# Performance work log

Measured on AMD Instinct MI355X. Metric: run time of the kernel, lower is better.

The kernel has to match this reference:

```python
import jax, jax.numpy as jnp
import numpy as np
from jax import lax

NAG = 3          # hardcoded in the torch module (query slices, catted_torches)
B = 4096         # batch_size per agent
H = 128          # hidden_dim
HEADS = 8
AD = H // HEADS  # attend_dim
STATE, ACT, SCAN = 48, 2, 256
OUTF, HID = 10, 256
NFEAT = 32 * (SCAN - 6)  # conv output features (two VALID convs: k5 then k3)
EPS = 1e-5

def leaky(x):
    return jnp.where(x >= 0, x, 0.01 * x)

def setup_inputs() -> dict:
    key = jax.random.key(0)
    ks = iter(jax.random.split(key, 40))
    def rn(shape, scale=0.05):
        return jax.random.normal(next(ks), shape, dtype=jnp.float32) * scale
    return {
        'obs':  jax.random.normal(next(ks), (NAG * B, STATE), jnp.float32),
        'acts': jax.random.normal(next(ks), (NAG * B, ACT), jnp.float32),
        'scan': jax.random.normal(next(ks), (NAG * B, SCAN), jnp.float32),
        'conv_w1': rn((32, 1, 5)),  'conv_b1': jnp.zeros((32,), jnp.float32),
        'conv_w2': rn((32, 32, 3)), 'conv_b2': jnp.zeros((32,), jnp.float32),
        'fc_w1': rn((256, NFEAT), 0.01), 'fc_b1': jnp.zeros((256,), jnp.float32),
        'fc_w2': rn((OUTF, 256)),        'fc_b2': jnp.zeros((OUTF,), jnp.float32),
        'enc_w': rn((H, STATE + ACT + OUTF)), 'enc_b': jnp.zeros((H,), jnp.float32),
        'Wk': rn((HEADS, AD, H)),
        'Wv': rn((HEADS, AD, H)), 'bv': jnp.zeros((HEADS, AD), jnp.float32),
        'Wq': rn((NAG, HEADS, AD, H)),
        'q1_w1': rn((HID, 2 * H)), 'q1_b1': jnp.zeros((HID,), jnp.float32),
        'q1_w2': rn((HID, HID)),   'q1_b2': jnp.zeros((HID,), jnp.float32),
        'q1_w3': rn((1, HID)),     'q1_b3': jnp.zeros((1,), jnp.float32),
        'q2_w1': rn((HID, 2 * H)), 'q2_b1': jnp.zeros((HID,), jnp.float32),
        'q2_w2': rn((HID, HID)),   'q2_b2': jnp.zeros((HID,), jnp.float32),
        'q2_w3': rn((1, HID)),     'q2_b3': jnp.zeros((1,), jnp.float32),
    }

def reference(obs, acts, scan, conv_w1, conv_b1, conv_w2, conv_b2,
              fc_w1, fc_b1, fc_w2, fc_b2, enc_w, enc_b, Wk, Wv, bv, Wq,
              q1_w1, q1_b1, q1_w2, q1_b2, q1_w3, q1_b3,
              q2_w1, q2_b1, q2_w2, q2_b2, q2_w3, q2_b3):
    dn = ('NCH', 'OIH', 'NCH')
    x = scan[:, None, :]                                            # [N,1,L]
    x = lax.conv_general_dilated(x, conv_w1, (1,), 'VALID', dimension_numbers=dn)
    x = jax.nn.relu(x + conv_b1[None, :, None])
    x = lax.conv_general_dilated(x, conv_w2, (1,), 'VALID', dimension_numbers=dn)
    x = jax.nn.relu(x + conv_b2[None, :, None])
    x = x.reshape(x.shape[0], -1)                                   # [N, NFEAT]
    x = jax.nn.relu(x @ fc_w1.T + fc_b1)
    feats = x @ fc_w2.T + fc_b2                                     # [N, OUTF]

    inps = jnp.concatenate([obs, acts, feats], axis=1)
    mu, var = inps.mean(0), inps.var(0)                             # BatchNorm1d (train, no affine)
    normed = (inps - mu) / jnp.sqrt(var + EPS)
    sa = leaky(normed @ enc_w.T + enc_b).reshape(NAG, B, H)         # [ag,B,H]

    keys = jnp.einsum('gbh,ndh->ngbd', sa, Wk)                      # [hd,ag,B,ad]
    vals = leaky(jnp.einsum('gbh,ndh->ngbd', sa, Wv) + bv[:, None, None, :])
    q = jnp.einsum('gbh,gndh->gnbd', sa, Wq)                        # [ag,hd,B,ad]

    logits = jnp.einsum('gnbd,nobd->gnbo', q, keys) / np.sqrt(AD)   # [ag,hd,B,ag]
    self_mask = jnp.eye(NAG, dtype=bool)[:, None, None, :]          # exclude own agent
    logits = jnp.where(self_mask, -jnp.inf, logits)
    w = jax.nn.softmax(logits, axis=-1)
    other = jnp.einsum('gnbo,nobd->gnbd', w, vals)                  # [ag,hd,B,ad]
    other = other.transpose(0, 2, 1, 3).reshape(NAG, B, H)          # heads concatenated

    emb = jnp.concatenate([sa, other], axis=2).reshape(NAG * B, 2 * H)

    def mlp(x, w1, b1, w2, b2, w3, b3):
        x = jax.nn.relu(x @ w1.T + b1)
        x = jax.nn.relu(x @ w2.T + b2)
        return x @ w3.T + b3

    q1 = mlp(emb, q1_w1, q1_b1, q1_w2, q1_b2, q1_w3, q1_b3)
    q2 = mlp(emb, q2_w1, q2_b1, q2_w2, q2_b2, q2_w3, q2_b3)
    return (q1, q2)
```

## Files before the change

### kernel.cpp

```cpp
#include <hip/hip_runtime.h>
#include <hip/hip_bf16.h>
#include <cstdint>
#include <cstddef>

typedef unsigned short u16;
typedef __attribute__((ext_vector_type(8))) __bf16 bf16x8;
typedef __attribute__((ext_vector_type(4))) float f32x4;

__device__ __forceinline__ u16 f2b(float f) {
  __hip_bfloat16 h = __float2bfloat16(f);
  return *reinterpret_cast<u16*>(&h);
}
__device__ __forceinline__ uint32_t pk2(float a, float b) {
  __hip_bfloat162 h = __float22bfloat162_rn(make_float2(a, b));
  return *reinterpret_cast<uint32_t*>(&h);
}
__device__ __forceinline__ float b2f(u16 u) {
  union { float f; uint32_t i; } x; x.i = ((uint32_t)u) << 16; return x.f;
}
__device__ __forceinline__ f32x4 mfma16(bf16x8 a, bf16x8 b, f32x4 c) {
  return __builtin_amdgcn_mfma_f32_16x16x32_bf16(a, b, c, 0, 0, 0);
}
__device__ __forceinline__ void async16(const void* g, void* l) {
  __builtin_amdgcn_global_load_lds((const __attribute__((address_space(1))) uint32_t*)g,
                                   (__attribute__((address_space(3))) uint32_t*)l, 16, 0, 0);
}

__global__ __launch_bounds__(256) void w1_perm(const float* __restrict__ w,
                                               u16* __restrict__ o) {
  __shared__ float L[8000];
  int j = blockIdx.x, tid = threadIdx.x;
  for (int i = tid; i < 8000; i += 256) L[i] = w[(size_t)j * 8000 + i];
  __syncthreads();
  for (int i = tid; i < 8000; i += 256) {
    int tt = i >> 5, c2 = i & 31;
    o[(size_t)j * 8000 + i] = f2b(L[c2 * 250 + tt]);
  }
}

struct CvtArgs {
  const float* src[13];
  void* dst[13];
  int cum[14];
  int kind[13];
};
__global__ __launch_bounds__(256) void f2b_multi(CvtArgs a, float* stats) {
  int i = blockIdx.x * 256 + threadIdx.x;
  if (blockIdx.x == 0 && threadIdx.x < 128) stats[threadIdx.x] = 0.f;
  int seg = 0;
  #pragma unroll
  for (int s = 1; s < 13; ++s) if (i >= a.cum[s]) seg = s;
  if (i < a.cum[13]) {
    int off = i - a.cum[seg];
    int kind = a.kind[seg];
    const float* src = a.src[seg];
    if (kind == 0) {
      ((u16*)a.dst[seg])[off] = f2b(src[off]);
    } else if (kind == 1) {
      int c2 = off / 96, rem = off - c2 * 96, kk = rem >> 5, c1 = rem & 31;
      ((u16*)a.dst[seg])[off] = f2b(src[(c2 * 32 + c1) * 3 + kk]);
    } else if (kind == 2) {
      int c1 = off >> 5, k = off & 31;
      ((u16*)a.dst[seg])[off] = f2b(k < 5 ? src[c1 * 5 + k] : 0.f);
    } else {
      ((float*)a.dst[seg])[off] = src[off];
    }
  }
}

__global__ __launch_bounds__(256) void conv_fused(
    const float* __restrict__ scan, const u16* __restrict__ w1g,
    const float* __restrict__ cb1, const u16* __restrict__ w2g,
    const float* __restrict__ cb2, u16* __restrict__ x, int row0) {
  __shared__ float s[260];
  __shared__ __align__(16) u16 A1[256 * 40];
  __shared__ __align__(16) u16 h1T[258 * 40];
  int tid = threadIdx.x;
  int lane = tid & 63, wv = tid >> 6;
  int l15 = lane & 15, quad = lane >> 4;
  s[tid] = scan[(size_t)(row0 + blockIdx.x) * 256 + tid];
  if (tid < 4) s[256 + tid] = 0.f;
  if (tid < 80) h1T[256 * 40 + tid] = 0;
  bf16x8 w1f[2];
  w1f[0] = *(const bf16x8*)&w1g[l15 * 32 + quad * 8];
  w1f[1] = *(const bf16x8*)&w1g[(16 + l15) * 32 + quad * 8];
  bf16x8 w2f[2][3];
  #pragma unroll
  for (int i = 0; i < 2; ++i)
    #pragma unroll
    for (int kk = 0; kk < 3; ++kk)
      w2f[i][kk] = *(const bf16x8*)&w2g[(i * 16 + l15) * 96 + kk * 32 + quad * 8];
  float cb1v[2][4], cb2v[2][4];
  #pragma unroll
  for (int i = 0; i < 2; ++i)
    #pragma unroll
    for (int r = 0; r < 4; ++r) {
      cb1v[i][r] = cb1[i * 16 + quad * 4 + r];
      cb2v[i][r] = cb2[i * 16 + quad * 4 + r];
    }
  __syncthreads();
  {
    union { bf16x8 v; u16 u[8]; } pk;
    #pragma unroll
    for (int k = 0; k < 5; ++k) pk.u[k] = f2b(s[tid + k]);
    pk.u[5] = 0; pk.u[6] = 0; pk.u[7] = 0;
    *(bf16x8*)&A1[tid * 40] = pk.v;
    uint4 z = make_uint4(0, 0, 0, 0);
    *(uint4*)&A1[tid * 40 + 8] = z;
    *(uint4*)&A1[tid * 40 + 16] = z;
    *(uint4*)&A1[tid * 40 + 24] = z;
  }
  __syncthreads();
  f32x4 zero = {0.f, 0.f, 0.f, 0.f};
  {
    f32x4 acc1[4][2];
    #pragma unroll
    for (int nt = 0; nt < 4; ++nt) { acc1[nt][0] = zero; acc1[nt][1] = zero; }
    #pragma unroll
    for (int nt = 0; nt < 4; ++nt) {
      int p = (wv * 4 + nt) * 16 + l15;
      bf16x8 bfr = *(const bf16x8*)&A1[p * 40 + quad * 8];
      acc1[nt][0] = mfma16(w1f[0], bfr, acc1[nt][0]);
      acc1[nt][1] = mfma16(w1f[1], bfr, acc1[nt][1]);
    }
    #pragma unroll
    for (int nt = 0; nt < 4; ++nt) {
      int p = (wv * 4 + nt) * 16 + l15;
      #pragma unroll
      for (int mt = 0; mt < 2; ++mt) {
        float v0 = fmaxf(acc1[nt][mt][0] + cb1v[mt][0], 0.f);
        float v1 = fmaxf(acc1[nt][mt][1] + cb1v[mt][1], 0.f);
        float v2 = fmaxf(acc1[nt][mt][2] + cb1v[mt][2], 0.f);
        float v3 = fmaxf(acc1[nt][mt][3] + cb1v[mt][3], 0.f);
        uint2 u; u.x = pk2(v0, v1); u.y = pk2(v2, v3);
        *(uint2*)&h1T[p * 40 + mt * 16 + quad * 4] = u;
      }
    }
  }
  __syncthreads();
  f32x4 acc2[4][2];
  #pragma unroll
  for (int jj = 0; jj < 4; ++jj) { acc2[jj][0] = zero; acc2[jj][1] = zero; }
  #pragma unroll
  for (int kk = 0; kk < 3; ++kk) {
    #pragma unroll
    for (int jj = 0; jj < 4; ++jj) {
      int t = (wv * 4 + jj) * 16 + l15 + kk;
      bf16x8 h = *(const bf16x8*)&h1T[t * 40 + quad * 8];
      acc2[jj][0] = mfma16(w2f[0][kk], h, acc2[jj][0]);
      acc2[jj][1] = mfma16(w2f[1][kk], h, acc2[jj][1]);
    }
  }
  u16* xr = x + (size_t)blockIdx.x * 8000;
  #pragma unroll
  for (int jj = 0; jj < 4; ++jj) {
    int t = (wv * 4 + jj) * 16 + l15;
    if (t < 250) {
      #pragma unroll
      for (int i = 0; i < 2; ++i) {
        float v0 = fmaxf(acc2[jj][i][0] + cb2v[i][0], 0.f);
        float v1 = fmaxf(acc2[jj][i][1] + cb2v[i][1], 0.f);
        float v2 = fmaxf(acc2[jj][i][2] + cb2v[i][2], 0.f);
        float v3 = fmaxf(acc2[jj][i][3] + cb2v[i][3], 0.f);
        uint2 u; u.x = pk2(v0, v1); u.y = pk2(v2, v3);
        *(uint2*)&xr[t * 32 + i * 16 + quad * 4] = u;
      }
    }
  }
}

template <int MODE>
__global__ __launch_bounds__(256) void gemm_bt(
    const u16* __restrict__ A, int lda, const u16* __restrict__ W, int ldw,
    const float* __restrict__ bias, float* __restrict__ outF,
    u16* __restrict__ outB, int ldo, int nst, int wq_sel, int a_sel,
    size_t out_zoff) {
  __shared__ __align__(16) u16 As[2][128 * 64];
  __shared__ __align__(16) u16 Bs[2][128 * 64];
  int tid = threadIdx.x;
  int m0 = blockIdx.y * 128, n0 = blockIdx.x * 128;
  if (wq_sel) W += (size_t)(blockIdx.y >> 5) * wq_sel;
  if (a_sel) A += (size_t)(blockIdx.x >> 1) * a_sel;
  int kbase = blockIdx.z * nst * 64;
  if (MODE == 0) outF += (size_t)blockIdx.z * out_zoff;
  const u16* Ap = A + (size_t)m0 * lda + kbase;
  const u16* Wp = W + (size_t)n0 * ldw + kbase;
  int lane = tid & 63, wv = tid >> 6;
  int l15 = lane & 15, quad = lane >> 4;
  int wm = (wv >> 1) * 64, wn = (wv & 1) * 64;
  f32x4 zero = {0.f, 0.f, 0.f, 0.f};
  f32x4 acc[4][4];
  #pragma unroll
  for (int i = 0; i < 4; ++i)
    #pragma unroll
    for (int j = 0; j < 4; ++j) acc[i][j] = zero;

  int srow[4], soff[4], sdst[4];
  #pragma unroll
  for (int it = 0; it < 4; ++it) {
    int c = it * 256 + tid;
    int row = c >> 3, slot = c & 7;
    srow[it] = row;
    soff[it] = ((slot ^ (row & 7)) * 8);
    sdst[it] = c * 8;
  }
  int rslot[2];
  rslot[0] = ((quad ^ (l15 & 7)) * 8);
  rslot[1] = (((4 + quad) ^ (l15 & 7)) * 8);

  #pragma unroll 1
  for (int st = 0; st < nst; ++st) {
    if (st == 0) {
      #pragma unroll
      for (int it = 0; it < 4; ++it) {
        async16(Ap + (size_t)srow[it] * lda + soff[it], &As[0][sdst[it]]);
        async16(Wp + (size_t)srow[it] * ldw + soff[it], &Bs[0][sdst[it]]);
      }
    }
    __syncthreads();
    if (st + 1 < nst) {
      const u16* An = Ap + (st + 1) * 64;
      const u16* Wn = Wp + (st + 1) * 64;
      u16* Ad = &As[(st + 1) & 1][0];
      u16* Bd = &Bs[(st + 1) & 1][0];
      #pragma unroll
      for (int it = 0; it < 4; ++it) {
        async16(An + (size_t)srow[it] * lda + soff[it], Ad + sdst[it]);
        async16(Wn + (size_t)srow[it] * ldw + soff[it], Bd + sdst[it]);
      }
    }
    const u16* Ab = &As[st & 1][0];
    const u16* Bb = &Bs[st & 1][0];
    #pragma unroll
    for (int s = 0; s < 2; ++s) {
      bf16x8 af[4], bfr[4];
      #pragma unroll
      for (int i = 0; i < 4; ++i)
        af[i] = *(const bf16x8*)&Ab[(wm + i * 16 + l15) * 64 + rslot[s]];
      #pragma unroll
      for (int j = 0; j < 4; ++j)
        bfr[j] = *(const bf16x8*)&Bb[(wn + j * 16 + l15) * 64 + rslot[s]];
      #pragma unroll
      for (int i = 0; i < 4; ++i)
        #pragma unroll
        for (int j = 0; j < 4; ++j) acc[i][j] = mfma16(af[i], bfr[j], acc[i][j]);
    }
  }
  #pragma unroll
  for (int i = 0; i < 4; ++i) {
    int mb = m0 + wm + i * 16 + quad * 4;
    #pragma unroll
    for (int j = 0; j < 4; ++j) {
      int n = n0 + wn + j * 16 + l15;
      float bv_ = (MODE == 1 || MODE == 2) ? bias[n] : 0.f;
      #pragma unroll
      for (int r = 0; r < 4; ++r) {
        float v = acc[i][j][r];
        if (MODE == 0) {
          outF[(size_t)(mb + r) * ldo + n] = v;
        } else {
          v += bv_;
          if (MODE == 1) v = fmaxf(v, 0.f);
          if (MODE == 2) v = v >= 0.f ? v : 0.01f * v;
          outB[(size_t)(mb + r) * ldo + n] = f2b(v);
        }
      }
    }
  }
}

__global__ __launch_bounds__(256) void fc2_stats(
    const float* __restrict__ hparts, const float* __restrict__ b1,
    const float* __restrict__ w2, const float* __restrict__ b2,
    const float* __restrict__ obs, const float* __restrict__ acts,
    float* __restrict__ inps, float* __restrict__ stats) {
  __shared__ float hL[32 * 260];
  __shared__ float w2L[10 * 260];
  __shared__ float b1L[256];
  __shared__ float ipL[32 * 61];
  int tid = threadIdx.x, r0 = blockIdx.x * 32;
  b1L[tid] = b1[tid];
  for (int i = tid; i < 2560; i += 256) w2L[(i >> 8) * 260 + (i & 255)] = w2[i];
  for (int i = tid; i < 32 * 48; i += 256) {
    int r = i / 48, f = i - r * 48;
    ipL[r * 61 + f] = obs[(size_t)(r0 + r) * 48 + f];
  }
  if (tid < 64) {
    int r = tid >> 1, f = tid & 1;
    ipL[r * 61 + 48 + f] = acts[(size_t)(r0 + r) * 2 + f];
  }
  __syncthreads();
  const size_t HS = (size_t)12288 * 256;
  for (int i = tid; i < 32 * 256; i += 256) {
    int r = i >> 8, c = i & 255;
    size_t g = (size_t)(r0 + r) * 256 + c;
    float v = b1L[c] + hparts[g] + hparts[g + HS] + hparts[g + 2 * HS] +
              hparts[g + 3 * HS] + hparts[g + 4 * HS];
    hL[r * 260 + c] = fmaxf(v, 0.f);
  }
  __syncthreads();
  {
    int r = tid >> 3, ob = tid & 7;
    for (int o = ob; o < 10; o += 8) {
      float a = 0.f;
      #pragma unroll 8
      for (int c = 0; c < 256; ++c) a += hL[r * 260 + c] * w2L[o * 260 + c];
      ipL[r * 61 + 50 + o] = a + b2[o];
    }
  }
  __syncthreads();
  for (int i = tid; i < 32 * 60; i += 256) {
    int r = i / 60, f = i - r * 60;
    inps[(size_t)(r0 + r) * 64 + f] = ipL[r * 61 + f];
  }
  if (tid < 60) {
    float s = 0.f, s2 = 0.f;
    for (int r = 0; r < 32; ++r) {
      float v = ipL[r * 61 + tid];
      s += v; s2 += v * v;
    }
    atomicAdd(&stats[tid], s);
    atomicAdd(&stats[64 + tid], s2);
  }
}

__global__ __launch_bounds__(256) void enc_kernel(
    const float* __restrict__ inps, const float* __restrict__ stats,
    const float* __restrict__ enc_w, const float* __restrict__ enc_b,
    u16* __restrict__ sab) {
  __shared__ float ewL[128 * 61];
  __shared__ float nrm[32 * 61];
  __shared__ float ebL[128];
  __shared__ float muL[60], ivL[60];
  int tid = threadIdx.x, r0 = blockIdx.x * 32;
  if (tid < 128) ebL[tid] = enc_b[tid];
  if (tid < 60) {
    float s = stats[tid], s2 = stats[64 + tid];
    float mu = s * (1.f / 12288.f);
    float var = s2 * (1.f / 12288.f) - mu * mu;
    muL[tid] = mu;
    ivL[tid] = rsqrtf(var + 1e-5f);
  }
  for (int i = tid; i < 128 * 60; i += 256) {
    int h = i / 60, f = i - h * 60;
    ewL[h * 61 + f] = enc_w[i];
  }
  __syncthreads();
  for (int i = tid; i < 32 * 60; i += 256) {
    int r = i / 60, f = i - r * 60;
    nrm[r * 61 + f] = (inps[(size_t)(r0 + r) * 64 + f] - muL[f]) * ivL[f];
  }
  __syncthreads();
  for (int i = tid; i < 32 * 128; i += 256) {
    int r = i >> 7, h = i & 127;
    float a = ebL[h];
    #pragma unroll 4
    for (int f = 0; f < 60; ++f) a += nrm[r * 61 + f] * ewL[h * 61 + f];
    a = a >= 0.f ? a : 0.01f * a;
    sab[(size_t)(r0 + r) * 128 + h] = f2b(a);
  }
}

__global__ __launch_bounds__(128) void attn_combine(
    const u16* __restrict__ qb, const u16* __restrict__ keysb,
    const u16* __restrict__ valsb, const u16* __restrict__ sab,
    u16* __restrict__ emb) {
  __shared__ float qL[3][128], kL[3][128], vL[3][128];
  __shared__ float lg[3][8][3], wgt[3][8][3];
  int b = blockIdx.x, t = threadIdx.x;
  #pragma unroll
  for (int o = 0; o < 3; ++o) {
    size_t base = (size_t)(o * 4096 + b) * 128 + t;
    qL[o][t] = b2f(qb[base]);
    kL[o][t] = b2f(keysb[base]);
    vL[o][t] = b2f(valsb[base]);
  }
  __syncthreads();
  if (t < 72) {
    int g = t / 24, n = (t / 3) % 8, o = t % 3;
    float a = 0.f;
    #pragma unroll
    for (int d = 0; d < 16; ++d) a += qL[g][n * 16 + d] * kL[o][n * 16 + d];
    lg[g][n][o] = (o == g) ? -1e30f : a * 0.25f;
  }
  __syncthreads();
  if (t < 24) {
    int g = t / 8, n = t % 8;
    float m = fmaxf(fmaxf(lg[g][n][0], lg[g][n][1]), lg[g][n][2]);
    float e0 = expf(lg[g][n][0] - m), e1 = expf(lg[g][n][1] - m),
          e2 = expf(lg[g][n][2] - m);
    float inv = 1.f / (e0 + e1 + e2);
    wgt[g][n][0] = e0 * inv; wgt[g][n][1] = e1 * inv; wgt[g][n][2] = e2 * inv;
  }
  __syncthreads();
  int n = t >> 4, d = t & 15;
  #pragma unroll
  for (int g = 0; g < 3; ++g) {
    float o_ = wgt[g][n][0] * vL[0][n * 16 + d] +
               wgt[g][n][1] * vL[1][n * 16 + d] +
               wgt[g][n][2] * vL[2][n * 16 + d];
    size_t rbase = (size_t)(g * 4096 + b) * 256;
    emb[rbase + 128 + t] = f2b(o_);
    emb[rbase + t] = sab[(size_t)(g * 4096 + b) * 128 + t];
  }
}

__global__ __launch_bounds__(256) void final_dot(
    const u16* __restrict__ t2ab, const float* __restrict__ w3a,
    const float* __restrict__ b3a, const float* __restrict__ w3b,
    const float* __restrict__ b3b, float* __restrict__ out) {
  int wv = threadIdx.x >> 6, lane = threadIdx.x & 63;
  int row = blockIdx.x * 4 + wv;
  float sa_ = 0.f, sb_ = 0.f;
  #pragma unroll
  for (int e = 0; e < 4; ++e) {
    int c = lane * 4 + e;
    sa_ += b2f(t2ab[(size_t)row * 512 + c]) * w3a[c];
    sb_ += b2f(t2ab[(size_t)row * 512 + 256 + c]) * w3b[c];
  }
  #pragma unroll
  for (int off = 32; off; off >>= 1) {
    sa_ += __shfl_down(sa_, off);
    sb_ += __shfl_down(sb_, off);
  }
  if (lane == 0) {
    out[row] = sa_ + b3a[0];
    out[12288 + row] = sb_ + b3b[0];
  }
}

extern "C" void kernel_launch(void* const* d_in, const int* in_sizes, int n_in,
                              void* d_out, int out_size, void* d_ws,
                              size_t ws_size, hipStream_t stream) {
  const float* obs  = (const float*)d_in[0];
  const float* acts = (const float*)d_in[1];
  const float* scan = (const float*)d_in[2];
  const float* cw1  = (const float*)d_in[3];
  const float* cb1  = (const float*)d_in[4];
  const float* cw2  = (const float*)d_in[5];
  const float* cb2  = (const float*)d_in[6];
  const float* fw1  = (const float*)d_in[7];
  const float* fb1  = (const float*)d_in[8];
  const float* fw2  = (const float*)d_in[9];
  const float* fb2  = (const float*)d_in[10];
  const float* encw = (const float*)d_in[11];
  const float* encb = (const float*)d_in[12];
  const float* Wk   = (const float*)d_in[13];
  const float* Wv   = (const float*)d_in[14];
  const float* bv   = (const float*)d_in[15];
  const float* Wq   = (const float*)d_in[16];
  const float* q1w1 = (const float*)d_in[17];
  const float* q1b1 = (const float*)d_in[18];
  const float* q1w2 = (const float*)d_in[19];
  const float* q1b2 = (const float*)d_in[20];
  const float* q1w3 = (const float*)d_in[21];
  const float* q1b3 = (const float*)d_in[22];
  const float* q2w1 = (const float*)d_in[23];
  const float* q2b1 = (const float*)d_in[24];
  const float* q2w2 = (const float*)d_in[25];
  const float* q2b2 = (const float*)d_in[26];
  const float* q2w3 = (const float*)d_in[27];
  const float* q2b3 = (const float*)d_in[28];
  float* out = (float*)d_out;
  char* ws = (char*)d_ws;
  if (ws_size < 166016000u) return;

  u16*   x     = (u16*)(ws + 0);
  u16*   w1b   = (u16*)(ws + 98304000);
  float* hpart = (float*)(ws + 102400000);
  float* stats = (float*)(ws + 165314560);
  u16*   wkb   = (u16*)(ws + 165315584);
  u16*   wvb   = (u16*)(ws + 165348352);
  u16*   wqb   = (u16*)(ws + 165381120);
  u16*   m1ab  = (u16*)(ws + 165479424);
  u16*   m2ab  = (u16*)(ws + 165741568);
  u16*   w2g   = (u16*)(ws + 166003712);
  u16*   w1g   = (u16*)(ws + 166009856);
  float* bc1   = (float*)(ws + 166011904);
  float* bc2   = (float*)(ws + 166013952);
  float* inps  = (float*)(ws + 0);
  u16*   sab   = (u16*)(ws + 3145728);
  u16*   keysb = (u16*)(ws + 6291456);
  u16*   valsb = (u16*)(ws + 9437184);
  u16*   qb    = (u16*)(ws + 12582912);
  u16*   embb  = (u16*)(ws + 15728640);
  u16*   t1ab  = (u16*)(ws + 22020096);
  u16*   t2ab  = (u16*)(ws + 34603008);

  w1_perm<<<256, 256, 0, stream>>>(fw1, w1b);
  CvtArgs ca;
  const float* srcs[13] = {Wk, Wv, Wq, q1w1, q2w1, q1w2, q2w2, cw2, cw1,
                           q1b1, q2b1, q1b2, q2b2};
  void* dsts[13] = {wkb, wvb, wqb, m1ab, m1ab + 65536, m2ab, m2ab + 65536,
                    w2g, w1g, bc1, bc1 + 256, bc2, bc2 + 256};
  const int sz[13] = {16384, 16384, 49152, 65536, 65536, 65536, 65536,
                      3072, 1024, 256, 256, 256, 256};
  const int kinds[13] = {0, 0, 0, 0, 0, 0, 0, 1, 2, 3, 3, 3, 3};
  int cum = 0;
  ca.cum[0] = 0;
  for (int i = 0; i < 13; ++i) {
    ca.src[i] = srcs[i]; ca.dst[i] = dsts[i]; ca.kind[i] = kinds[i];
    cum += sz[i]; ca.cum[i + 1] = cum;
  }
  f2b_multi<<<(cum + 255) / 256, 256, 0, stream>>>(ca, stats);

  for (int s = 0; s < 2; ++s) {
    conv_fused<<<6144, 256, 0, stream>>>(scan, w1g, cb1, w2g, cb2, x, s * 6144);
    gemm_bt<0><<<dim3(2, 48, 5), 256, 0, stream>>>(
        x, 8000, w1b, 8000, nullptr, hpart + (size_t)s * 6144 * 256, nullptr,
        256, 25, 0, 0, (size_t)12288 * 256);
  }
  fc2_stats<<<384, 256, 0, stream>>>(hpart, fb1, fw2, fb2, obs, acts, inps, stats);
  enc_kernel<<<384, 256, 0, stream>>>(inps, stats, encw, encb, sab);
  gemm_bt<3><<<dim3(1, 96, 1), 256, 0, stream>>>(sab, 128, wkb, 128, nullptr,
                                                 nullptr, keysb, 128, 2, 0, 0, 0);
  gemm_bt<2><<<dim3(1, 96, 1), 256, 0, stream>>>(sab, 128, wvb, 128, bv, nullptr,
                                                 valsb, 128, 2, 0, 0, 0);
  gemm_bt<3><<<dim3(1, 96, 1), 256, 0, stream>>>(sab, 128, wqb, 128, nullptr,
                                                 nullptr, qb, 128, 2, 16384, 0, 0);
  attn_combine<<<4096, 128, 0, stream>>>(qb, keysb, valsb, sab, embb);
  gemm_bt<1><<<dim3(4, 96, 1), 256, 0, stream>>>(embb, 256, m1ab, 256, bc1,
                                                 nullptr, t1ab, 512, 4, 0, 0, 0);
  gemm_bt<1><<<dim3(4, 96, 1), 256, 0, stream>>>(t1ab, 512, m2ab, 256, bc2,
                                                 nullptr, t2ab, 512, 4, 0, 256, 0);
  final_dot<<<3072, 256, 0, stream>>>(t2ab, q1w3, q1b3, q2w3, q2b3, out);
}
```

Baseline: 358.2 us.

## Halve GEMM K-tile to 32 and slim conv LDS staging with zero buffer

The shared GEMM kernel's K-stage shrinks from 64 to 32, halving LDS use (64KB to 32KB per block) with a matching swizzle, and every launch's stage count is doubled to cover the same K. This should allow more blocks per CU, in exchange for twice as many barriers and loop iterations per tile. The conv kernel drops its float staging buffer and padded A1 layout. Each thread now reads its five scan taps straight from global memory, and lanes with quad>0 read a shared zero row, which removes two __syncthreads and the zero-fill stores. The conv change relies on wave-local LDS visibility, ordered only by an s_waitcnt, since each wave reads only the A1 rows it wrote itself.

```diff
diff --git a/kernel.cpp b/kernel.cpp
--- a/kernel.cpp
+++ b/kernel.cpp
@@ -72,14 +72,25 @@
     const float* __restrict__ scan, const u16* __restrict__ w1g,
     const float* __restrict__ cb1, const u16* __restrict__ w2g,
     const float* __restrict__ cb2, u16* __restrict__ x, int row0) {
-  __shared__ float s[260];
-  __shared__ __align__(16) u16 A1[256 * 40];
+  __shared__ __align__(16) u16 A1[256 * 8];
+  __shared__ __align__(16) u16 zbuf[4 * 8];
   __shared__ __align__(16) u16 h1T[258 * 40];
   int tid = threadIdx.x;
   int lane = tid & 63, wv = tid >> 6;
   int l15 = lane & 15, quad = lane >> 4;
-  s[tid] = scan[(size_t)(row0 + blockIdx.x) * 256 + tid];
-  if (tid < 4) s[256 + tid] = 0.f;
+  const float* srow = scan + (size_t)(row0 + blockIdx.x) * 256;
+  float sv[5];
+  #pragma unroll
+  for (int k = 0; k < 5; ++k) {
+    int p = tid + k;
+    sv[k] = (p < 256) ? srow[p] : 0.f;
+  }
+  union { bf16x8 v; u16 u[8]; } pk_;
+  #pragma unroll
+  for (int k = 0; k < 5; ++k) pk_.u[k] = f2b(sv[k]);
+  pk_.u[5] = 0; pk_.u[6] = 0; pk_.u[7] = 0;
+  *(bf16x8*)&A1[tid * 8] = pk_.v;
+  if (lane < 8) zbuf[wv * 8 + lane] = 0;
   if (tid < 80) h1T[256 * 40 + tid] = 0;
   bf16x8 w1f[2];
   w1f[0] = *(const bf16x8*)&w1g[l15 * 32 + quad * 8];
@@ -98,19 +109,7 @@
       cb1v[i][r] = cb1[i * 16 + quad * 4 + r];
       cb2v[i][r] = cb2[i * 16 + quad * 4 + r];
     }
-  __syncthreads();
-  {
-    union { bf16x8 v; u16 u[8]; } pk;
-    #pragma unroll
-    for (int k = 0; k < 5; ++k) pk.u[k] = f2b(s[tid + k]);
-    pk.u[5] = 0; pk.u[6] = 0; pk.u[7] = 0;
-    *(bf16x8*)&A1[tid * 40] = pk.v;
-    uint4 z = make_uint4(0, 0, 0, 0);
-    *(uint4*)&A1[tid * 40 + 8] = z;
-    *(uint4*)&A1[tid * 40 + 16] = z;
-    *(uint4*)&A1[tid * 40 + 24] = z;
-  }
-  __syncthreads();
+  asm volatile("s_waitcnt lgkmcnt(0)" ::: "memory");
   f32x4 zero = {0.f, 0.f, 0.f, 0.f};
   {
     f32x4 acc1[4][2];
@@ -119,7 +118,8 @@
     #pragma unroll
     for (int nt = 0; nt < 4; ++nt) {
       int p = (wv * 4 + nt) * 16 + l15;
-      bf16x8 bfr = *(const bf16x8*)&A1[p * 40 + quad * 8];
+      const u16* bp = (quad == 0) ? &A1[p * 8] : &zbuf[wv * 8];
+      bf16x8 bfr = *(const bf16x8*)bp;
       acc1[nt][0] = mfma16(w1f[0], bfr, acc1[nt][0]);
       acc1[nt][1] = mfma16(w1f[1], bfr, acc1[nt][1]);
     }
@@ -175,13 +175,13 @@
     const float* __restrict__ bias, float* __restrict__ outF,
     u16* __restrict__ outB, int ldo, int nst, int wq_sel, int a_sel,
     size_t out_zoff) {
-  __shared__ __align__(16) u16 As[2][128 * 64];
-  __shared__ __align__(16) u16 Bs[2][128 * 64];
+  __shared__ __align__(16) u16 As[2][128 * 32];
+  __shared__ __align__(16) u16 Bs[2][128 * 32];
   int tid = threadIdx.x;
   int m0 = blockIdx.y * 128, n0 = blockIdx.x * 128;
   if (wq_sel) W += (size_t)(blockIdx.y >> 5) * wq_sel;
   if (a_sel) A += (size_t)(blockIdx.x >> 1) * a_sel;
-  int kbase = blockIdx.z * nst * 64;
+  int kbase = blockIdx.z * nst * 32;
   if (MODE == 0) outF += (size_t)blockIdx.z * out_zoff;
   const u16* Ap = A + (size_t)m0 * lda + kbase;
   const u16* Wp = W + (size_t)n0 * ldw + kbase;
@@ -195,56 +195,51 @@
     #pragma unroll
     for (int j = 0; j < 4; ++j) acc[i][j] = zero;
 
-  int srow[4], soff[4], sdst[4];
-  #pragma unroll
-  for (int it = 0; it < 4; ++it) {
+  int srow[2], soff[2], sdst[2];
+  #pragma unroll
+  for (int it = 0; it < 2; ++it) {
     int c = it * 256 + tid;
-    int row = c >> 3, slot = c & 7;
+    int row = c >> 2, slot = c & 3;
     srow[it] = row;
-    soff[it] = ((slot ^ (row & 7)) * 8);
+    soff[it] = ((slot ^ (row & 3)) * 8);
     sdst[it] = c * 8;
   }
-  int rslot[2];
-  rslot[0] = ((quad ^ (l15 & 7)) * 8);
-  rslot[1] = (((4 + quad) ^ (l15 & 7)) * 8);
+  int rslot = ((quad ^ (l15 & 3)) * 8);
 
   #pragma unroll 1
   for (int st = 0; st < nst; ++st) {
     if (st == 0) {
       #pragma unroll
-      for (int it = 0; it < 4; ++it) {
+      for (int it = 0; it < 2; ++it) {
         async16(Ap + (size_t)srow[it] * lda + soff[it], &As[0][sdst[it]]);
         async16(Wp + (size_t)srow[it] * ldw + soff[it], &Bs[0][sdst[it]]);
       }
     }
     __syncthreads();
     if (st + 1 < nst) {
-      const u16* An = Ap + (st + 1) * 64;
-      const u16* Wn = Wp + (st + 1) * 64;
+      const u16* An = Ap + (st + 1) * 32;
+      const u16* Wn = Wp + (st + 1) * 32;
       u16* Ad = &As[(st + 1) & 1][0];
       u16* Bd = &Bs[(st + 1) & 1][0];
       #pragma unroll
-      for (int it = 0; it < 4; ++it) {
+      for (int it = 0; it < 2; ++it) {
         async16(An + (size_t)srow[it] * lda + soff[it], Ad + sdst[it]);
         async16(Wn + (size_t)srow[it] * ldw + soff[it], Bd + sdst[it]);
       }
     }
     const u16* Ab = &As[st & 1][0];
     const u16* Bb = &Bs[st & 1][0];
-    #pragma unroll
-    for (int s = 0; s < 2; ++s) {
-      bf16x8 af[4], bfr[4];
+    bf16x8 af[4], bfr[4];
+    #pragma unroll
+    for (int i = 0; i < 4; ++i)
+      af[i] = *(const bf16x8*)&Ab[(wm + i * 16 + l15) * 32 + rslot];
+    #pragma unroll
+    for (int j = 0; j < 4; ++j)
+      bfr[j] = *(const bf16x8*)&Bb[(wn + j * 16 + l15) * 32 + rslot];
+    #pragma unroll
+    for (int i = 0; i < 4; ++i)
       #pragma unroll
-      for (int i = 0; i < 4; ++i)
-        af[i] = *(const bf16x8*)&Ab[(wm + i * 16 + l15) * 64 + rslot[s]];
-      #pragma unroll
-      for (int j = 0; j < 4; ++j)
-        bfr[j] = *(const bf16x8*)&Bb[(wn + j * 16 + l15) * 64 + rslot[s]];
-      #pragma unroll
-      for (int i = 0; i < 4; ++i)
-        #pragma unroll
-        for (int j = 0; j < 4; ++j) acc[i][j] = mfma16(af[i], bfr[j], acc[i][j]);
-    }
+      for (int j = 0; j < 4; ++j) acc[i][j] = mfma16(af[i], bfr[j], acc[i][j]);
   }
   #pragma unroll
   for (int i = 0; i < 4; ++i) {
@@ -508,20 +503,20 @@
     conv_fused<<<6144, 256, 0, stream>>>(scan, w1g, cb1, w2g, cb2, x, s * 6144);
     gemm_bt<0><<<dim3(2, 48, 5), 256, 0, stream>>>(
         x, 8000, w1b, 8000, nullptr, hpart + (size_t)s * 6144 * 256, nullptr,
-        256, 25, 0, 0, (size_t)12288 * 256);
+        256, 50, 0, 0, (size_t)12288 * 256);
   }
   fc2_stats<<<384, 256, 0, stream>>>(hpart, fb1, fw2, fb2, obs, acts, inps, stats);
   enc_kernel<<<384, 256, 0, stream>>>(inps, stats, encw, encb, sab);
   gemm_bt<3><<<dim3(1, 96, 1), 256, 0, stream>>>(sab, 128, wkb, 128, nullptr,
-                                                 nullptr, keysb, 128, 2, 0, 0, 0);
+                                                 nullptr, keysb, 128, 4, 0, 0, 0);
   gemm_bt<2><<<dim3(1, 96, 1), 256, 0, stream>>>(sab, 128, wvb, 128, bv, nullptr,
-                                                 valsb, 128, 2, 0, 0, 0);
+                                                 valsb, 128, 4, 0, 0, 0);
   gemm_bt<3><<<dim3(1, 96, 1), 256, 0, stream>>>(sab, 128, wqb, 128, nullptr,
-                                                 nullptr, qb, 128, 2, 16384, 0, 0);
+                                                 nullptr, qb, 128, 4, 16384, 0, 0);
   attn_combine<<<4096, 128, 0, stream>>>(qb, keysb, valsb, sab, embb);
   gemm_bt<1><<<dim3(4, 96, 1), 256, 0, stream>>>(embb, 256, m1ab, 256, bc1,
-                                                 nullptr, t1ab, 512, 4, 0, 0, 0);
+                                                 nullptr, t1ab, 512, 8, 0, 0, 0);
   gemm_bt<1><<<dim3(4, 96, 1), 256, 0, stream>>>(t1ab, 512, m2ab, 256, bc2,
-                                                 nullptr, t2ab, 512, 4, 0, 256, 0);
+                                                 nullptr, t2ab, 512, 8, 0, 256, 0);
   final_dot<<<3072, 256, 0, stream>>>(t2ab, q1w3, q1b3, q2w3, q2b3, out);
 }
```

New measurement: 380.8 us. 1.06x slower.

## Restructure conv kernel per-wave rows, fuse K/V/Q GEMMs, use 64-row GEMM tiles

Applied to the files above, without the earlier changes.

The conv kernel now gives each wave its own 64-position slice, with private LDS and no block barriers, and loops over 4 rows per block. It also reads scan directly from global memory and feeds the K=32 MFMA from a shared zero buffer for the padded quads. The conv and fc1 GEMM now run over all 12288 rows in one pass instead of two halves, which doubles the workspace. The K, V and Q projections are merged into one launch (MODE 4), and every GEMM uses 64-row M tiles so more blocks are in flight, at the cost of less reuse per block.

```diff
diff --git a/kernel.cpp b/kernel.cpp
--- a/kernel.cpp
+++ b/kernel.cpp
@@ -71,16 +71,12 @@
 __global__ __launch_bounds__(256) void conv_fused(
     const float* __restrict__ scan, const u16* __restrict__ w1g,
     const float* __restrict__ cb1, const u16* __restrict__ w2g,
-    const float* __restrict__ cb2, u16* __restrict__ x, int row0) {
-  __shared__ float s[260];
-  __shared__ __align__(16) u16 A1[256 * 40];
-  __shared__ __align__(16) u16 h1T[258 * 40];
-  int tid = threadIdx.x;
-  int lane = tid & 63, wv = tid >> 6;
+    const float* __restrict__ cb2, u16* __restrict__ x) {
+  __shared__ __align__(16) u16 A1[4][80 * 8];
+  __shared__ __align__(16) u16 zb[4][8];
+  __shared__ __align__(16) u16 h1[4][80 * 40];
+  int tid = threadIdx.x, lane = tid & 63, wv = tid >> 6;
   int l15 = lane & 15, quad = lane >> 4;
-  s[tid] = scan[(size_t)(row0 + blockIdx.x) * 256 + tid];
-  if (tid < 4) s[256 + tid] = 0.f;
-  if (tid < 80) h1T[256 * 40 + tid] = 0;
   bf16x8 w1f[2];
   w1f[0] = *(const bf16x8*)&w1g[l15 * 32 + quad * 8];
   w1f[1] = *(const bf16x8*)&w1g[(16 + l15) * 32 + quad * 8];
@@ -98,34 +94,53 @@
       cb1v[i][r] = cb1[i * 16 + quad * 4 + r];
       cb2v[i][r] = cb2[i * 16 + quad * 4 + r];
     }
-  __syncthreads();
-  {
-    union { bf16x8 v; u16 u[8]; } pk;
-    #pragma unroll
-    for (int k = 0; k < 5; ++k) pk.u[k] = f2b(s[tid + k]);
-    pk.u[5] = 0; pk.u[6] = 0; pk.u[7] = 0;
-    *(bf16x8*)&A1[tid * 40] = pk.v;
-    uint4 z = make_uint4(0, 0, 0, 0);
-    *(uint4*)&A1[tid * 40 + 8] = z;
-    *(uint4*)&A1[tid * 40 + 16] = z;
-    *(uint4*)&A1[tid * 40 + 24] = z;
-  }
-  __syncthreads();
+  if (lane < 8) zb[wv][lane] = 0;
+  u16* A1w = &A1[wv][0];
+  u16* h1w = &h1[wv][0];
+  int p0 = wv * 64;
   f32x4 zero = {0.f, 0.f, 0.f, 0.f};
-  {
-    f32x4 acc1[4][2];
-    #pragma unroll
-    for (int nt = 0; nt < 4; ++nt) { acc1[nt][0] = zero; acc1[nt][1] = zero; }
-    #pragma unroll
-    for (int nt = 0; nt < 4; ++nt) {
-      int p = (wv * 4 + nt) * 16 + l15;
-      bf16x8 bfr = *(const bf16x8*)&A1[p * 40 + quad * 8];
+  #pragma unroll 1
+  for (int rr = 0; rr < 4; ++rr) {
+    int row = blockIdx.x * 4 + rr;
+    const float* srow = scan + (size_t)row * 256;
+    asm volatile("s_waitcnt lgkmcnt(0)" ::: "memory");
+    {
+      union { bf16x8 v; u16 u[8]; } pk_;
+      int gp = p0 + lane;
+      #pragma unroll
+      for (int k = 0; k < 5; ++k) {
+        int p = gp + k;
+        pk_.u[k] = f2b(p < 256 ? srow[p] : 0.f);
+      }
+      pk_.u[5] = 0; pk_.u[6] = 0; pk_.u[7] = 0;
+      *(bf16x8*)&A1w[lane * 8] = pk_.v;
+      if (lane < 16) {
+        union { bf16x8 v; u16 u[8]; } pq_;
+        gp = p0 + 64 + lane;
+        #pragma unroll
+        for (int k = 0; k < 5; ++k) {
+          int p = gp + k;
+          pq_.u[k] = f2b(p < 256 ? srow[p] : 0.f);
+        }
+        pq_.u[5] = 0; pq_.u[6] = 0; pq_.u[7] = 0;
+        *(bf16x8*)&A1w[(64 + lane) * 8] = pq_.v;
+      }
+    }
+    asm volatile("s_waitcnt lgkmcnt(0)" ::: "memory");
+    f32x4 acc1[5][2];
+    #pragma unroll
+    for (int nt = 0; nt < 5; ++nt) { acc1[nt][0] = zero; acc1[nt][1] = zero; }
+    #pragma unroll
+    for (int nt = 0; nt < 5; ++nt) {
+      int lr = nt * 16 + l15;
+      const u16* bp = (quad == 0) ? &A1w[lr * 8] : &zb[wv][0];
+      bf16x8 bfr = *(const bf16x8*)bp;
       acc1[nt][0] = mfma16(w1f[0], bfr, acc1[nt][0]);
       acc1[nt][1] = mfma16(w1f[1], bfr, acc1[nt][1]);
     }
     #pragma unroll
-    for (int nt = 0; nt < 4; ++nt) {
-      int p = (wv * 4 + nt) * 16 + l15;
+    for (int nt = 0; nt < 5; ++nt) {
+      int lr = nt * 16 + l15;
       #pragma unroll
       for (int mt = 0; mt < 2; ++mt) {
         float v0 = fmaxf(acc1[nt][mt][0] + cb1v[mt][0], 0.f);
@@ -133,53 +148,59 @@
         float v2 = fmaxf(acc1[nt][mt][2] + cb1v[mt][2], 0.f);
         float v3 = fmaxf(acc1[nt][mt][3] + cb1v[mt][3], 0.f);
         uint2 u; u.x = pk2(v0, v1); u.y = pk2(v2, v3);
-        *(uint2*)&h1T[p * 40 + mt * 16 + quad * 4] = u;
+        *(uint2*)&h1w[lr * 40 + mt * 16 + quad * 4] = u;
       }
     }
-  }
-  __syncthreads();
-  f32x4 acc2[4][2];
-  #pragma unroll
-  for (int jj = 0; jj < 4; ++jj) { acc2[jj][0] = zero; acc2[jj][1] = zero; }
-  #pragma unroll
-  for (int kk = 0; kk < 3; ++kk) {
+    asm volatile("s_waitcnt lgkmcnt(0)" ::: "memory");
+    f32x4 acc2[4][2];
+    #pragma unroll
+    for (int jj = 0; jj < 4; ++jj) { acc2[jj][0] = zero; acc2[jj][1] = zero; }
+    #pragma unroll
+    for (int kk = 0; kk < 3; ++kk) {
+      #pragma unroll
+      for (int jj = 0; jj < 4; ++jj) {
+        int lt = jj * 16 + l15 + kk;
+        bf16x8 h = *(const bf16x8*)&h1w[lt * 40 + quad * 8];
+        acc2[jj][0] = mfma16(w2f[0][kk], h, acc2[jj][0]);
+        acc2[jj][1] = mfma16(w2f[1][kk], h, acc2[jj][1]);
+      }
+    }
+    u16* xr = x + (size_t)row * 8000;
     #pragma unroll
     for (int jj = 0; jj < 4; ++jj) {
-      int t = (wv * 4 + jj) * 16 + l15 + kk;
-      bf16x8 h = *(const bf16x8*)&h1T[t * 40 + quad * 8];
-      acc2[jj][0] = mfma16(w2f[0][kk], h, acc2[jj][0]);
-      acc2[jj][1] = mfma16(w2f[1][kk], h, acc2[jj][1]);
-    }
-  }
-  u16* xr = x + (size_t)blockIdx.x * 8000;
-  #pragma unroll
-  for (int jj = 0; jj < 4; ++jj) {
-    int t = (wv * 4 + jj) * 16 + l15;
-    if (t < 250) {
-      #pragma unroll
-      for (int i = 0; i < 2; ++i) {
-        float v0 = fmaxf(acc2[jj][i][0] + cb2v[i][0], 0.f);
-        float v1 = fmaxf(acc2[jj][i][1] + cb2v[i][1], 0.f);
-        float v2 = fmaxf(acc2[jj][i][2] + cb2v[i][2], 0.f);
-        float v3 = fmaxf(acc2[jj][i][3] + cb2v[i][3], 0.f);
-        uint2 u; u.x = pk2(v0, v1); u.y = pk2(v2, v3);
-        *(uint2*)&xr[t * 32 + i * 16 + quad * 4] = u;
+      int t = p0 + jj * 16 + l15;
+      if (t < 250) {
+        #pragma unroll
+        for (int i = 0; i < 2; ++i) {
+          float v0 = fmaxf(acc2[jj][i][0] + cb2v[i][0], 0.f);
+          float v1 = fmaxf(acc2[jj][i][1] + cb2v[i][1], 0.f);
+          float v2 = fmaxf(acc2[jj][i][2] + cb2v[i][2], 0.f);
+          float v3 = fmaxf(acc2[jj][i][3] + cb2v[i][3], 0.f);
+          uint2 u; u.x = pk2(v0, v1); u.y = pk2(v2, v3);
+          *(uint2*)&xr[t * 32 + i * 16 + quad * 4] = u;
+        }
       }
     }
   }
 }
 
-template <int MODE>
+template <int MODE, int MROWS>
 __global__ __launch_bounds__(256) void gemm_bt(
     const u16* __restrict__ A, int lda, const u16* __restrict__ W, int ldw,
     const float* __restrict__ bias, float* __restrict__ outF,
-    u16* __restrict__ outB, int ldo, int nst, int wq_sel, int a_sel,
-    size_t out_zoff) {
-  __shared__ __align__(16) u16 As[2][128 * 64];
+    u16* __restrict__ outB, int ldo, int nst, int a_sel, size_t out_zoff) {
+  constexpr int AI = (MROWS * 8) / 256;
+  __shared__ __align__(16) u16 As[2][MROWS * 64];
   __shared__ __align__(16) u16 Bs[2][128 * 64];
   int tid = threadIdx.x;
-  int m0 = blockIdx.y * 128, n0 = blockIdx.x * 128;
-  if (wq_sel) W += (size_t)(blockIdx.y >> 5) * wq_sel;
+  int m0 = blockIdx.y * MROWS;
+  int sel = (MODE == 4) ? blockIdx.x : 0;
+  int n0 = (MODE == 4) ? 0 : blockIdx.x * 128;
+  if (MODE == 4) {
+    size_t woff = (sel < 2) ? (size_t)sel * 128 : (size_t)(256 + (m0 >> 12) * 128);
+    W += woff * 128;
+    outB += (size_t)sel * 12288 * 128;
+  }
   if (a_sel) A += (size_t)(blockIdx.x >> 1) * a_sel;
   int kbase = blockIdx.z * nst * 64;
   if (MODE == 0) outF += (size_t)blockIdx.z * out_zoff;
@@ -187,22 +208,32 @@
   const u16* Wp = W + (size_t)n0 * ldw + kbase;
   int lane = tid & 63, wv = tid >> 6;
   int l15 = lane & 15, quad = lane >> 4;
-  int wm = (wv >> 1) * 64, wn = (wv & 1) * 64;
+  int wm = (wv >> 1) * (MROWS / 2), wn = (wv & 1) * 64;
+  constexpr int MI = MROWS / 32;
   f32x4 zero = {0.f, 0.f, 0.f, 0.f};
-  f32x4 acc[4][4];
-  #pragma unroll
-  for (int i = 0; i < 4; ++i)
+  f32x4 acc[MI][4];
+  #pragma unroll
+  for (int i = 0; i < MI; ++i)
     #pragma unroll
     for (int j = 0; j < 4; ++j) acc[i][j] = zero;
 
-  int srow[4], soff[4], sdst[4];
+  int sraA[AI], sofA[AI], sdsA[AI];
+  #pragma unroll
+  for (int it = 0; it < AI; ++it) {
+    int c = it * 256 + tid;
+    int row = c >> 3, slot = c & 7;
+    sraA[it] = row;
+    sofA[it] = ((slot ^ (row & 7)) * 8);
+    sdsA[it] = c * 8;
+  }
+  int sraW[4], sofW[4], sdsW[4];
   #pragma unroll
   for (int it = 0; it < 4; ++it) {
     int c = it * 256 + tid;
     int row = c >> 3, slot = c & 7;
-    srow[it] = row;
-    soff[it] = ((slot ^ (row & 7)) * 8);
-    sdst[it] = c * 8;
+    sraW[it] = row;
+    sofW[it] = ((slot ^ (row & 7)) * 8);
+    sdsW[it] = c * 8;
   }
   int rslot[2];
   rslot[0] = ((quad ^ (l15 & 7)) * 8);
@@ -212,10 +243,11 @@
   for (int st = 0; st < nst; ++st) {
     if (st == 0) {
       #pragma unroll
-      for (int it = 0; it < 4; ++it) {
-        async16(Ap + (size_t)srow[it] * lda + soff[it], &As[0][sdst[it]]);
-        async16(Wp + (size_t)srow[it] * ldw + soff[it], &Bs[0][sdst[it]]);
-      }
+      for (int it = 0; it < AI; ++it)
+        async16(Ap + (size_t)sraA[it] * lda + sofA[it], &As[0][sdsA[it]]);
+      #pragma unroll
+      for (int it = 0; it < 4; ++it)
+        async16(Wp + (size_t)sraW[it] * ldw + sofW[it], &Bs[0][sdsW[it]]);
     }
     __syncthreads();
     if (st + 1 < nst) {
@@ -224,44 +256,46 @@
       u16* Ad = &As[(st + 1) & 1][0];
       u16* Bd = &Bs[(st + 1) & 1][0];
       #pragma unroll
-      for (int it = 0; it < 4; ++it) {
-        async16(An + (size_t)srow[it] * lda + soff[it], Ad + sdst[it]);
-        async16(Wn + (size_t)srow[it] * ldw + soff[it], Bd + sdst[it]);
-      }
+      for (int it = 0; it < AI; ++it)
+        async16(An + (size_t)sraA[it] * lda + sofA[it], Ad + sdsA[it]);
+      #pragma unroll
+      for (int it = 0; it < 4; ++it)
+        async16(Wn + (size_t)sraW[it] * ldw + sofW[it], Bd + sdsW[it]);
     }
     const u16* Ab = &As[st & 1][0];
     const u16* Bb = &Bs[st & 1][0];
     #pragma unroll
     for (int s = 0; s < 2; ++s) {
-      bf16x8 af[4], bfr[4];
-      #pragma unroll
-      for (int i = 0; i < 4; ++i)
+      bf16x8 af[MI], bfr[4];
+      #pragma unroll
+      for (int i = 0; i < MI; ++i)
         af[i] = *(const bf16x8*)&Ab[(wm + i * 16 + l15) * 64 + rslot[s]];
       #pragma unroll
       for (int j = 0; j < 4; ++j)
         bfr[j] = *(const bf16x8*)&Bb[(wn + j * 16 + l15) * 64 + rslot[s]];
       #pragma unroll
-      for (int i = 0; i < 4; ++i)
+      for (int i = 0; i < MI; ++i)
         #pragma unroll
         for (int j = 0; j < 4; ++j) acc[i][j] = mfma16(af[i], bfr[j], acc[i][j]);
     }
   }
   #pragma unroll
-  for (int i = 0; i < 4; ++i) {
+  for (int i = 0; i < MI; ++i) {
     int mb = m0 + wm + i * 16 + quad * 4;
     #pragma unroll
     for (int j = 0; j < 4; ++j) {
       int n = n0 + wn + j * 16 + l15;
-      float bv_ = (MODE == 1 || MODE == 2) ? bias[n] : 0.f;
+      float bv_ = (MODE == 1 || MODE == 4) ? bias[n] : 0.f;
       #pragma unroll
       for (int r = 0; r < 4; ++r) {
         float v = acc[i][j][r];
         if (MODE == 0) {
           outF[(size_t)(mb + r) * ldo + n] = v;
+        } else if (MODE == 1) {
+          v = fmaxf(v + bv_, 0.f);
+          outB[(size_t)(mb + r) * ldo + n] = f2b(v);
         } else {
-          v += bv_;
-          if (MODE == 1) v = fmaxf(v, 0.f);
-          if (MODE == 2) v = v >= 0.f ? v : 0.01f * v;
+          if (sel == 1) { v += bv_; v = v >= 0.f ? v : 0.01f * v; }
           outB[(size_t)(mb + r) * ldo + n] = f2b(v);
         }
       }
@@ -463,36 +497,35 @@
   const float* q2b3 = (const float*)d_in[28];
   float* out = (float*)d_out;
   char* ws = (char*)d_ws;
-  if (ws_size < 166016000u) return;
+  if (ws_size < 264400000u) return;
 
   u16*   x     = (u16*)(ws + 0);
-  u16*   w1b   = (u16*)(ws + 98304000);
-  float* hpart = (float*)(ws + 102400000);
-  float* stats = (float*)(ws + 165314560);
-  u16*   wkb   = (u16*)(ws + 165315584);
-  u16*   wvb   = (u16*)(ws + 165348352);
-  u16*   wqb   = (u16*)(ws + 165381120);
-  u16*   m1ab  = (u16*)(ws + 165479424);
-  u16*   m2ab  = (u16*)(ws + 165741568);
-  u16*   w2g   = (u16*)(ws + 166003712);
-  u16*   w1g   = (u16*)(ws + 166009856);
-  float* bc1   = (float*)(ws + 166011904);
-  float* bc2   = (float*)(ws + 166013952);
+  u16*   w1b   = (u16*)(ws + 196608000);
+  float* hpart = (float*)(ws + 200704000);
+  float* stats = (float*)(ws + 263618560);
+  u16*   wkvqb = (u16*)(ws + 263619584);
+  u16*   m1ab  = (u16*)(ws + 263783424);
+  u16*   m2ab  = (u16*)(ws + 264045568);
+  u16*   w2g   = (u16*)(ws + 264307712);
+  u16*   w1g   = (u16*)(ws + 264313856);
+  float* bc1   = (float*)(ws + 264315904);
+  float* bc2   = (float*)(ws + 264317952);
   float* inps  = (float*)(ws + 0);
   u16*   sab   = (u16*)(ws + 3145728);
-  u16*   keysb = (u16*)(ws + 6291456);
-  u16*   valsb = (u16*)(ws + 9437184);
-  u16*   qb    = (u16*)(ws + 12582912);
+  u16*   kvqb  = (u16*)(ws + 6291456);
   u16*   embb  = (u16*)(ws + 15728640);
   u16*   t1ab  = (u16*)(ws + 22020096);
   u16*   t2ab  = (u16*)(ws + 34603008);
+  u16*   keysb = kvqb;
+  u16*   valsb = kvqb + (size_t)12288 * 128;
+  u16*   qb    = kvqb + (size_t)2 * 12288 * 128;
 
   w1_perm<<<256, 256, 0, stream>>>(fw1, w1b);
   CvtArgs ca;
   const float* srcs[13] = {Wk, Wv, Wq, q1w1, q2w1, q1w2, q2w2, cw2, cw1,
                            q1b1, q2b1, q1b2, q2b2};
-  void* dsts[13] = {wkb, wvb, wqb, m1ab, m1ab + 65536, m2ab, m2ab + 65536,
-                    w2g, w1g, bc1, bc1 + 256, bc2, bc2 + 256};
+  void* dsts[13] = {wkvqb, wkvqb + 16384, wkvqb + 32768, m1ab, m1ab + 65536,
+                    m2ab, m2ab + 65536, w2g, w1g, bc1, bc1 + 256, bc2, bc2 + 256};
   const int sz[13] = {16384, 16384, 49152, 65536, 65536, 65536, 65536,
                       3072, 1024, 256, 256, 256, 256};
   const int kinds[13] = {0, 0, 0, 0, 0, 0, 0, 1, 2, 3, 3, 3, 3};
@@ -504,24 +537,18 @@
   }
   f2b_multi<<<(cum + 255) / 256, 256, 0, stream>>>(ca, stats);
 
-  for (int s = 0; s < 2; ++s) {
-    conv_fused<<<6144, 256, 0, stream>>>(scan, w1g, cb1, w2g, cb2, x, s * 6144);
-    gemm_bt<0><<<dim3(2, 48, 5), 256, 0, stream>>>(
-        x, 8000, w1b, 8000, nullptr, hpart + (size_t)s * 6144 * 256, nullptr,
-        256, 25, 0, 0, (size_t)12288 * 256);
-  }
+  conv_fused<<<3072, 256, 0, stream>>>(scan, w1g, cb1, w2g, cb2, x);
+  gemm_bt<0, 64><<<dim3(2, 192, 5), 256, 0, stream>>>(
+      x, 8000, w1b, 8000, nullptr, hpart, nullptr, 256, 25, 0,
+      (size_t)12288 * 256);
   fc2_stats<<<384, 256, 0, stream>>>(hpart, fb1, fw2, fb2, obs, acts, inps, stats);
   enc_kernel<<<384, 256, 0, stream>>>(inps, stats, encw, encb, sab);
-  gemm_bt<3><<<dim3(1, 96, 1), 256, 0, stream>>>(sab, 128, wkb, 128, nullptr,
-                                                 nullptr, keysb, 128, 2, 0, 0, 0);
-  gemm_bt<2><<<dim3(1, 96, 1), 256, 0, stream>>>(sab, 128, wvb, 128, bv, nullptr,
-                                                 valsb, 128, 2, 0, 0, 0);
-  gemm_bt<3><<<dim3(1, 96, 1), 256, 0, stream>>>(sab, 128, wqb, 128, nullptr,
-                                                 nullptr, qb, 128, 2, 16384, 0, 0);
+  gemm_bt<4, 64><<<dim3(3, 192, 1), 256, 0, stream>>>(
+      sab, 128, wkvqb, 128, bv, nullptr, kvqb, 128, 2, 0, 0);
   attn_combine<<<4096, 128, 0, stream>>>(qb, keysb, valsb, sab, embb);
-  gemm_bt<1><<<dim3(4, 96, 1), 256, 0, stream>>>(embb, 256, m1ab, 256, bc1,
-                                                 nullptr, t1ab, 512, 4, 0, 0, 0);
-  gemm_bt<1><<<dim3(4, 96, 1), 256, 0, stream>>>(t1ab, 512, m2ab, 256, bc2,
-                                                 nullptr, t2ab, 512, 4, 0, 256, 0);
+  gemm_bt<1, 64><<<dim3(4, 192, 1), 256, 0, stream>>>(
+      embb, 256, m1ab, 256, bc1, nullptr, t1ab, 512, 4, 0, 0);
+  gemm_bt<1, 64><<<dim3(4, 192, 1), 256, 0, stream>>>(
+      t1ab, 512, m2ab, 256, bc2, nullptr, t2ab, 512, 4, 256, 0);
   final_dot<<<3072, 256, 0, stream>>>(t2ab, q1w3, q1b3, q2w3, q2b3, out);
 }
```

Result: slower. 385.3 us (+7.6%).
